# Kernel optimization log

Measured on AMD Instinct MI355X. Metric: run time of the kernel, lower is better.

Reference implementation:

```python
import jax, jax.numpy as jnp
import numpy as np

N_HEAD = 16
K_SPARSE = 16

def setup_inputs() -> dict:
    key = jax.random.key(0)
    k1, k2, k3, k4 = jax.random.split(key, 4)
    B, T, C = 4, 1024, 1024
    x = jax.random.normal(k1, (B, T, C), dtype=jnp.float32)
    W_attn = jax.random.normal(k2, (3 * C, C), dtype=jnp.float32) * 0.02
    W_proj = jax.random.normal(k3, (C, C), dtype=jnp.float32) * 0.02
    W_rel = jax.random.normal(k4, (N_HEAD, C), dtype=jnp.float32) * 0.02
    return {"x": x, "W_attn": W_attn, "W_proj": W_proj, "W_rel": W_rel}


def reference(x, W_attn, W_proj, W_rel):
    B, T, C = x.shape
    H = W_rel.shape[0]
    hd = C // H
    K = min(K_SPARSE, T)

    # qkv projection (no bias): [B,T,3C] -> three [B,H,T,hd]
    qkv = x @ W_attn.T
    q, k, v = jnp.split(qkv, 3, axis=-1)
    q = q.reshape(B, T, H, hd).transpose(0, 2, 1, 3)
    k = k.reshape(B, T, H, hd).transpose(0, 2, 1, 3)
    v = v.reshape(B, T, H, hd).transpose(0, 2, 1, 3)

    # per-head relevance scores of batch 0 (original indexes top_indices[0]),
    # masked with row 0 of the causal tril (original uses masked_relevance[:, 0, :]):
    # only position 0 keeps a finite score.
    rel = jnp.einsum('tc,hc->ht', x[0], W_rel)              # [H,T]
    s = jnp.where(jnp.arange(T) == 0, rel, -jnp.inf)         # [H,T]

    t_ar = jnp.arange(T)
    # per-query masking (j <= t) then top-k routing per (head, t)
    scores = jnp.where(t_ar[:, None] >= t_ar[None, :], s[:, None, :], -jnp.inf)  # [H,T,T]
    _, idx = jax.lax.top_k(scores, K)                        # [H,T,K]
    slots = jnp.arange(K)
    # for t+1 <= K the original uses arange(t+1) (valid slots masked below)
    idx = jnp.where((t_ar < K)[None, :, None], slots[None, None, :], idx)
    valid = slots[None, :] <= t_ar[:, None]                  # [T,K]

    # gather selected keys / values: [B,H,T,K,hd]
    h_ix = jnp.arange(H)[:, None, None]
    k_sel = k[:, h_ix, idx]
    v_sel = v[:, h_ix, idx]

    logits = jnp.einsum('bhtd,bhtkd->bhtk', q, k_sel) / jnp.sqrt(jnp.float32(hd))
    logits = jnp.where(valid[None, None], logits, -jnp.inf)
    w = jax.nn.softmax(logits, axis=-1)                      # dropout = identity (eval)
    out = jnp.einsum('bhtk,bhtkd->bhtd', w, v_sel)

    out = out.transpose(0, 2, 1, 3).reshape(B, T, C)
    return out @ W_proj.T
```

## Files before the change

### kernel.cpp

```cpp
#include <hip/hip_runtime.h>
#include <hip/hip_bf16.h>
#include <stdint.h>

typedef __bf16 bf16x8 __attribute__((ext_vector_type(8)));
typedef float  f32x4  __attribute__((ext_vector_type(4)));

constexpr int Bb = 4;
constexpr int Tt = 1024;
constexpr int Cc = 1024;
constexpr int Kk = 16;
constexpr int HK = 256;

__device__ inline __bf16 f2bf(float f) {
    union { __hip_bfloat16 h; __bf16 b; } u;
    u.h = __float2bfloat16(f);
    return u.b;
}

__device__ inline void load_lds16(const void* g, void* l) {
    auto gp = (const __attribute__((address_space(1))) unsigned int*)(uintptr_t)g;
    auto lp = (__attribute__((address_space(3))) unsigned int*)(uintptr_t)l;
    __builtin_amdgcn_global_load_lds(gp, lp, 16, 0, 0);
}

__device__ inline bf16x8 frag_f32(const float* p) {
    f32x4 lo = *reinterpret_cast<const f32x4*>(p);
    f32x4 hi = *reinterpret_cast<const f32x4*>(p + 4);
    bf16x8 r;
    r[0] = f2bf(lo[0]); r[1] = f2bf(lo[1]); r[2] = f2bf(lo[2]); r[3] = f2bf(lo[3]);
    r[4] = f2bf(hi[0]); r[5] = f2bf(hi[1]); r[6] = f2bf(hi[2]); r[7] = f2bf(hi[3]);
    return r;
}

__global__ __launch_bounds__(256)
void kv_gemm(const float* __restrict__ x, const float* __restrict__ Wkv,
             float* __restrict__ kv_part)
{
    __shared__ float As[64 * 32];
    __shared__ float Bs[64 * 32];
    const int lane = threadIdx.x & 63;
    const int wave = threadIdx.x >> 6;
    const int wm = wave >> 1, wn = wave & 1;
    const int tileN = blockIdx.x * 64;
    const int kz = blockIdx.z;
    const int r16 = lane & 15;
    const int kq  = (lane >> 4) * 8;

    f32x4 acc[2][2] = {};
    for (int kk = kz * 256; kk < kz * 256 + 256; kk += 32) {
#pragma unroll
        for (int t = 0; t < 2; ++t) {
            int g = (wave * 2 + t) * 64 + lane;
            int r = g >> 3;
            int colf = (g & 7) * 4;
            size_t grow = (size_t)(r >> 4) * Tt + (r & 15);
            load_lds16(x + grow * (size_t)Cc + kk + colf, As + (wave * 2 + t) * 256);
            load_lds16(Wkv + (size_t)(tileN + r) * Cc + kk + colf, Bs + (wave * 2 + t) * 256);
        }
        __syncthreads();
        bf16x8 a[2], b[2];
#pragma unroll
        for (int i = 0; i < 2; ++i) {
            a[i] = frag_f32(As + (wm * 32 + i * 16 + r16) * 32 + kq);
            b[i] = frag_f32(Bs + (wn * 32 + i * 16 + r16) * 32 + kq);
        }
#pragma unroll
        for (int i = 0; i < 2; ++i)
#pragma unroll
            for (int j = 0; j < 2; ++j)
                acc[i][j] = __builtin_amdgcn_mfma_f32_16x16x32_bf16(a[i], b[j], acc[i][j], 0, 0, 0);
        __syncthreads();
    }

    const int crow0 = (lane >> 4) * 4;
    const int ccol  = lane & 15;
    float* outp = kv_part + (size_t)kz * 64 * 2048;
#pragma unroll
    for (int i = 0; i < 2; ++i)
#pragma unroll
        for (int j = 0; j < 2; ++j)
#pragma unroll
            for (int r = 0; r < 4; ++r)
                outp[(size_t)(wm * 32 + i * 16 + crow0 + r) * 2048
                     + tileN + wn * 32 + j * 16 + ccol] = acc[i][j][r];
}

__global__ __launch_bounds__(256)
void precompute(const float* __restrict__ kv_part,
                const float* __restrict__ W_attn,
                const float* __restrict__ W_proj,
                __hip_bfloat16* __restrict__ QKb,
                __hip_bfloat16* __restrict__ vPt)
{
    __shared__ float sel[64][16];
    const int blk = blockIdx.x;
    const int type = blk >> 8;
    const int bh = (blk >> 2) & 63;
    const int cchunk = blk & 3;
    const int b = bh >> 4, h = bh & 15;
    const int tid = threadIdx.x;

    for (int e = tid; e < Kk * 64; e += 256) {
        int k = e >> 6, d = e & 63;
        size_t off = (size_t)(b * Kk + k) * 2048 + type * 1024 + h * 64 + d;
        float s = kv_part[off] + kv_part[off + 64 * 2048]
                + kv_part[off + 2 * 64 * 2048] + kv_part[off + 3 * 64 * 2048];
        sel[d][k] = s;
    }
    __syncthreads();

    const int c = cchunk * 256 + tid;
    float acc[Kk] = {};

    if (type == 0) {
        const float* wp = W_attn + (size_t)(h * 64) * 1024 + c;
#pragma unroll 4
        for (int d = 0; d < 64; ++d) {
            float wv = wp[(size_t)d * 1024];
            const float4* sv = reinterpret_cast<const float4*>(sel[d]);
            float4 s0 = sv[0], s1 = sv[1], s2 = sv[2], s3 = sv[3];
            acc[0]  += wv * s0.x; acc[1]  += wv * s0.y; acc[2]  += wv * s0.z; acc[3]  += wv * s0.w;
            acc[4]  += wv * s1.x; acc[5]  += wv * s1.y; acc[6]  += wv * s1.z; acc[7]  += wv * s1.w;
            acc[8]  += wv * s2.x; acc[9]  += wv * s2.y; acc[10] += wv * s2.z; acc[11] += wv * s2.w;
            acc[12] += wv * s3.x; acc[13] += wv * s3.y; acc[14] += wv * s3.z; acc[15] += wv * s3.w;
        }
#pragma unroll
        for (int k = 0; k < Kk; ++k)
            QKb[((size_t)b * HK + h * 16 + k) * 1024 + c] = __float2bfloat16(acc[k]);
    } else {
        const float* wrow = W_proj + (size_t)c * 1024 + h * 64;
#pragma unroll 4
        for (int d4 = 0; d4 < 64; d4 += 4) {
            float4 wv = *reinterpret_cast<const float4*>(wrow + d4);
            const float w4[4] = {wv.x, wv.y, wv.z, wv.w};
#pragma unroll
            for (int dd = 0; dd < 4; ++dd) {
                float wvv = w4[dd];
                const float4* sv = reinterpret_cast<const float4*>(sel[d4 + dd]);
                float4 s0 = sv[0], s1 = sv[1], s2 = sv[2], s3 = sv[3];
                acc[0]  += wvv * s0.x; acc[1]  += wvv * s0.y; acc[2]  += wvv * s0.z; acc[3]  += wvv * s0.w;
                acc[4]  += wvv * s1.x; acc[5]  += wvv * s1.y; acc[6]  += wvv * s1.z; acc[7]  += wvv * s1.w;
                acc[8]  += wvv * s2.x; acc[9]  += wvv * s2.y; acc[10] += wvv * s2.z; acc[11] += wvv * s2.w;
                acc[12] += wvv * s3.x; acc[13] += wvv * s3.y; acc[14] += wvv * s3.z; acc[15] += wvv * s3.w;
            }
        }
        bf16x8 p0, p1;
#pragma unroll
        for (int k = 0; k < 8; ++k) { p0[k] = f2bf(acc[k]); p1[k] = f2bf(acc[k + 8]); }
        __hip_bfloat16* dst = vPt + ((size_t)b * 1024 + c) * HK + h * 16;
        *reinterpret_cast<bf16x8*>(dst) = p0;
        *reinterpret_cast<bf16x8*>(dst + 8) = p1;
    }
}

__global__ __launch_bounds__(256)
void logits_softmax(const float* __restrict__ x,
                    const __hip_bfloat16* __restrict__ QKb,
                    __hip_bfloat16* __restrict__ wout)
{
    __shared__ float As[32 * 32];
    __shared__ __hip_bfloat16 Bs[64 * 32];

    const float* A = x + (size_t)blockIdx.z * Tt * Cc;
    const __hip_bfloat16* Bm = QKb + (size_t)blockIdx.z * HK * Cc;

    const int lane = threadIdx.x & 63;
    const int wave = threadIdx.x >> 6;
    const int wm = wave >> 1, wn = wave & 1;
    const int tileM = blockIdx.y * 32;
    const int tileN = blockIdx.x * 64;
    const int r16 = lane & 15;
    const int kq  = (lane >> 4) * 8;

    f32x4 acc[2] = {};
    for (int kk = 0; kk < Cc; kk += 32) {
        {
            int g = wave * 64 + lane;
            load_lds16(A + (size_t)(tileM + (g >> 3)) * Cc + kk + (g & 7) * 4,
                       As + wave * 256);
        }
        {
            int g = wave * 64 + lane;
            load_lds16(Bm + (size_t)(tileN + (g >> 2)) * Cc + kk + (g & 3) * 8,
                       Bs + wave * 512);
        }
        __syncthreads();
        bf16x8 a = frag_f32(As + (wm * 16 + r16) * 32 + kq);
        bf16x8 b[2];
#pragma unroll
        for (int j = 0; j < 2; ++j)
            b[j] = *reinterpret_cast<const bf16x8*>(Bs + (size_t)(wn * 32 + j * 16 + r16) * 32 + kq);
#pragma unroll
        for (int j = 0; j < 2; ++j)
            acc[j] = __builtin_amdgcn_mfma_f32_16x16x32_bf16(a, b[j], acc[j], 0, 0, 0);
        __syncthreads();
    }

    const int crow0 = (lane >> 4) * 4;
    const int ccol  = lane & 15;
#pragma unroll
    for (int r = 0; r < 4; ++r) {
        int t = tileM + wm * 16 + crow0 + r;
        bool valid = (ccol <= t);
#pragma unroll
        for (int j = 0; j < 2; ++j) {
            int hk = tileN + wn * 32 + j * 16 + ccol;
            float v = acc[j][r] * 0.125f;
            float vm = valid ? v : -3.0e38f;
#pragma unroll
            for (int m = 1; m < 16; m <<= 1) vm = fmaxf(vm, __shfl_xor(vm, m));
            float e = valid ? __expf(v - vm) : 0.f;
            float s = e;
#pragma unroll
            for (int m = 1; m < 16; m <<= 1) s += __shfl_xor(s, m);
            wout[((size_t)blockIdx.z * Tt + t) * HK + hk] = __float2bfloat16(e / s);
        }
    }
}

__global__ __launch_bounds__(256)
void out_gemm(const __hip_bfloat16* __restrict__ Aw,
              const __hip_bfloat16* __restrict__ Bv,
              float* __restrict__ Cout)
{
    constexpr int BM = 128, BN = 64;
    __shared__ __hip_bfloat16 smem[(BM + BN) * 32];
    __hip_bfloat16* As = smem;
    __hip_bfloat16* Bs = smem + BM * 32;

    const __hip_bfloat16* A = Aw + (size_t)blockIdx.z * Tt * HK;
    const __hip_bfloat16* Bm = Bv + (size_t)blockIdx.z * Cc * HK;

    const int lane = threadIdx.x & 63;
    const int wave = threadIdx.x >> 6;
    const int wm = wave >> 1, wn = wave & 1;
    const int tileM = blockIdx.y * BM;
    const int tileN = blockIdx.x * BN;
    const int r16 = lane & 15;
    const int kq  = (lane >> 4) * 8;

    f32x4 acc[4][2] = {};
    for (int kk = 0; kk < HK; kk += 32) {
#pragma unroll
        for (int t = 0; t < BM / 64; ++t) {
            int g = (wave * (BM / 64) + t) * 64 + lane;
            load_lds16(A + (size_t)(tileM + (g >> 2)) * HK + kk + (g & 3) * 8,
                       As + (size_t)(wave * (BM / 64) + t) * 512);
        }
        {
            int g = wave * 64 + lane;
            load_lds16(Bm + (size_t)(tileN + (g >> 2)) * HK + kk + (g & 3) * 8,
                       Bs + (size_t)wave * 512);
        }
        __syncthreads();
        bf16x8 a[4], b[2];
#pragma unroll
        for (int i = 0; i < 4; ++i)
            a[i] = *reinterpret_cast<const bf16x8*>(
                As + (size_t)(wm * 64 + i * 16 + r16) * 32 + kq);
#pragma unroll
        for (int j = 0; j < 2; ++j)
            b[j] = *reinterpret_cast<const bf16x8*>(
                Bs + (size_t)(wn * 32 + j * 16 + r16) * 32 + kq);
#pragma unroll
        for (int i = 0; i < 4; ++i)
#pragma unroll
            for (int j = 0; j < 2; ++j)
                acc[i][j] = __builtin_amdgcn_mfma_f32_16x16x32_bf16(a[i], b[j], acc[i][j], 0, 0, 0);
        __syncthreads();
    }

    const int crow0 = (lane >> 4) * 4;
    const int ccol  = lane & 15;
    float* outp = Cout + (size_t)blockIdx.z * Tt * Cc;
#pragma unroll
    for (int i = 0; i < 4; ++i)
#pragma unroll
        for (int j = 0; j < 2; ++j)
#pragma unroll
            for (int r = 0; r < 4; ++r)
                outp[(size_t)(tileM + wm * 64 + i * 16 + crow0 + r) * Cc
                     + tileN + wn * 32 + j * 16 + ccol] = acc[i][j][r];
}

extern "C" void kernel_launch(void* const* d_in, const int* in_sizes, int n_in,
                              void* d_out, int out_size, void* d_ws, size_t ws_size,
                              hipStream_t stream)
{
    (void)in_sizes; (void)n_in; (void)out_size; (void)ws_size;
    const float* x      = (const float*)d_in[0];
    const float* W_attn = (const float*)d_in[1];
    const float* W_proj = (const float*)d_in[2];
    float* out = (float*)d_out;

    char* ws = (char*)d_ws;
    float*          kv_part = (float*)ws;
    __hip_bfloat16* QKb  = (__hip_bfloat16*)(ws + (2u << 20));
    __hip_bfloat16* vPt  = (__hip_bfloat16*)(ws + (4u << 20));
    __hip_bfloat16* w_ws = (__hip_bfloat16*)(ws + (6u << 20));

    kv_gemm<<<dim3(32, 1, 4), 256, 0, stream>>>(x, W_attn + (size_t)Cc * Cc, kv_part);
    precompute<<<512, 256, 0, stream>>>(kv_part, W_attn, W_proj, QKb, vPt);
    logits_softmax<<<dim3(HK / 64, Tt / 32, Bb), 256, 0, stream>>>(x, QKb, w_ws);
    out_gemm<<<dim3(Cc / 64, Tt / 128, Bb), 256, 0, stream>>>(w_ws, vPt, out);
}
```

Baseline: 124.1 us.

## Convert fp32 operands to bf16 once when staging to LDS, deepen K step

Both GEMM kernels now convert fp32 inputs to bf16 in registers as they are staged into LDS, instead of streaming fp32 into LDS via global_load_lds and converting per fragment read. The LDS rows are padded to 40 elements to reduce bank conflicts. logits_softmax also processes 64 K-columns per iteration, halving the number of syncs. The projection kernel's unroll factor rises from 4 to 8. The cost is a register round-trip for the A-operand loads, which loses the asynchronous direct-to-LDS path.

```diff
diff --git a/kernel.cpp b/kernel.cpp
--- a/kernel.cpp
+++ b/kernel.cpp
@@ -23,7 +23,7 @@
     __builtin_amdgcn_global_load_lds(gp, lp, 16, 0, 0);
 }
 
-__device__ inline bf16x8 frag_f32(const float* p) {
+__device__ inline bf16x8 cvt8(const float* p) {
     f32x4 lo = *reinterpret_cast<const f32x4*>(p);
     f32x4 hi = *reinterpret_cast<const f32x4*>(p + 4);
     bf16x8 r;
@@ -36,33 +36,30 @@
 void kv_gemm(const float* __restrict__ x, const float* __restrict__ Wkv,
              float* __restrict__ kv_part)
 {
-    __shared__ float As[64 * 32];
-    __shared__ float Bs[64 * 32];
-    const int lane = threadIdx.x & 63;
-    const int wave = threadIdx.x >> 6;
+    __shared__ __hip_bfloat16 As[64 * 40];
+    __shared__ __hip_bfloat16 Bs[64 * 40];
+    const int tid = threadIdx.x;
+    const int lane = tid & 63;
+    const int wave = tid >> 6;
     const int wm = wave >> 1, wn = wave & 1;
     const int tileN = blockIdx.x * 64;
     const int kz = blockIdx.z;
     const int r16 = lane & 15;
     const int kq  = (lane >> 4) * 8;
 
+    const int sr = tid >> 2, sc = (tid & 3) * 8;
+    const size_t arow = (size_t)(sr >> 4) * Tt + (sr & 15);
+
     f32x4 acc[2][2] = {};
     for (int kk = kz * 256; kk < kz * 256 + 256; kk += 32) {
-#pragma unroll
-        for (int t = 0; t < 2; ++t) {
-            int g = (wave * 2 + t) * 64 + lane;
-            int r = g >> 3;
-            int colf = (g & 7) * 4;
-            size_t grow = (size_t)(r >> 4) * Tt + (r & 15);
-            load_lds16(x + grow * (size_t)Cc + kk + colf, As + (wave * 2 + t) * 256);
-            load_lds16(Wkv + (size_t)(tileN + r) * Cc + kk + colf, Bs + (wave * 2 + t) * 256);
-        }
+        *reinterpret_cast<bf16x8*>(As + sr * 40 + sc) = cvt8(x + arow * Cc + kk + sc);
+        *reinterpret_cast<bf16x8*>(Bs + sr * 40 + sc) = cvt8(Wkv + (size_t)(tileN + sr) * Cc + kk + sc);
         __syncthreads();
         bf16x8 a[2], b[2];
 #pragma unroll
         for (int i = 0; i < 2; ++i) {
-            a[i] = frag_f32(As + (wm * 32 + i * 16 + r16) * 32 + kq);
-            b[i] = frag_f32(Bs + (wn * 32 + i * 16 + r16) * 32 + kq);
+            a[i] = *reinterpret_cast<const bf16x8*>(As + (wm * 32 + i * 16 + r16) * 40 + kq);
+            b[i] = *reinterpret_cast<const bf16x8*>(Bs + (wn * 32 + i * 16 + r16) * 40 + kq);
         }
 #pragma unroll
         for (int i = 0; i < 2; ++i)
@@ -114,7 +111,7 @@
 
     if (type == 0) {
         const float* wp = W_attn + (size_t)(h * 64) * 1024 + c;
-#pragma unroll 4
+#pragma unroll 8
         for (int d = 0; d < 64; ++d) {
             float wv = wp[(size_t)d * 1024];
             const float4* sv = reinterpret_cast<const float4*>(sel[d]);
@@ -129,7 +126,7 @@
             QKb[((size_t)b * HK + h * 16 + k) * 1024 + c] = __float2bfloat16(acc[k]);
     } else {
         const float* wrow = W_proj + (size_t)c * 1024 + h * 64;
-#pragma unroll 4
+#pragma unroll 8
         for (int d4 = 0; d4 < 64; d4 += 4) {
             float4 wv = *reinterpret_cast<const float4*>(wrow + d4);
             const float w4[4] = {wv.x, wv.y, wv.z, wv.w};
@@ -158,41 +155,50 @@
                     const __hip_bfloat16* __restrict__ QKb,
                     __hip_bfloat16* __restrict__ wout)
 {
-    __shared__ float As[32 * 32];
-    __shared__ __hip_bfloat16 Bs[64 * 32];
+    __shared__ __hip_bfloat16 Ah[2][32 * 40];
+    __shared__ __hip_bfloat16 Bh[2][64 * 32];
 
     const float* A = x + (size_t)blockIdx.z * Tt * Cc;
     const __hip_bfloat16* Bm = QKb + (size_t)blockIdx.z * HK * Cc;
 
-    const int lane = threadIdx.x & 63;
-    const int wave = threadIdx.x >> 6;
+    const int tid = threadIdx.x;
+    const int lane = tid & 63;
+    const int wave = tid >> 6;
     const int wm = wave >> 1, wn = wave & 1;
     const int tileM = blockIdx.y * 32;
     const int tileN = blockIdx.x * 64;
     const int r16 = lane & 15;
     const int kq  = (lane >> 4) * 8;
 
+    const int ar = tid >> 3, ac = (tid & 7) * 8;
+    const int ahalf = ac >> 5, acol = ac & 31;
+
     f32x4 acc[2] = {};
-    for (int kk = 0; kk < Cc; kk += 32) {
-        {
+    for (int kk = 0; kk < Cc; kk += 64) {
+#pragma unroll
+        for (int h = 0; h < 2; ++h) {
             int g = wave * 64 + lane;
-            load_lds16(A + (size_t)(tileM + (g >> 3)) * Cc + kk + (g & 7) * 4,
-                       As + wave * 256);
-        }
-        {
-            int g = wave * 64 + lane;
-            load_lds16(Bm + (size_t)(tileN + (g >> 2)) * Cc + kk + (g & 3) * 8,
-                       Bs + wave * 512);
-        }
-        __syncthreads();
-        bf16x8 a = frag_f32(As + (wm * 16 + r16) * 32 + kq);
-        bf16x8 b[2];
-#pragma unroll
-        for (int j = 0; j < 2; ++j)
-            b[j] = *reinterpret_cast<const bf16x8*>(Bs + (size_t)(wn * 32 + j * 16 + r16) * 32 + kq);
-#pragma unroll
-        for (int j = 0; j < 2; ++j)
-            acc[j] = __builtin_amdgcn_mfma_f32_16x16x32_bf16(a, b[j], acc[j], 0, 0, 0);
+            load_lds16(Bm + (size_t)(tileN + (g >> 2)) * Cc + kk + h * 32 + (g & 3) * 8,
+                       &Bh[h][0] + wave * 512);
+        }
+        *reinterpret_cast<bf16x8*>(&Ah[ahalf][0] + ar * 40 + acol) =
+            cvt8(A + (size_t)(tileM + ar) * Cc + kk + ac);
+        __syncthreads();
+
+        bf16x8 a[2], b[2][2];
+#pragma unroll
+        for (int s = 0; s < 2; ++s) {
+            a[s] = *reinterpret_cast<const bf16x8*>(&Ah[s][0] + (wm * 16 + r16) * 40 + kq);
+#pragma unroll
+            for (int j = 0; j < 2; ++j)
+                b[s][j] = *reinterpret_cast<const bf16x8*>(
+                    &Bh[s][0] + (wn * 32 + j * 16 + r16) * 32 + kq);
+        }
+#pragma unroll
+        for (int s = 0; s < 2; ++s)
+#pragma unroll
+            for (int j = 0; j < 2; ++j)
+                acc[j] = __builtin_amdgcn_mfma_f32_16x16x32_bf16(a[s], b[s][j], acc[j], 0, 0, 0);
         __syncthreads();
     }
 
```

New measurement: 121.5 us. 1.02x faster.
